# Performance work log

Measured on AMD Instinct MI355X. Metric: run time of the kernel, lower is better.

Reference implementation:

```python
import jax, jax.numpy as jnp
import numpy as np

FS = 16000
NUM_BANDS = 15
CENTER_FREQ = 150
FFT_SIZE = 512
FFT_IN = 256
HOP = 128
NUM_FRAMES = 30
BETA = 1.0 + 10.0 ** (15.0 / 20.0)
FFT_PAD = (FFT_SIZE - FFT_IN) // 2
ROWS = FFT_SIZE // 2 + 1


def _make_fftmat():
    window = np.hanning(FFT_IN)
    window = np.concatenate([np.zeros(FFT_PAD), window, np.zeros(FFT_PAD)])
    fft = np.fft.fft(np.eye(FFT_SIZE))
    fft = np.vstack((np.real(fft[:ROWS, :]), np.imag(fft[:ROWS, :])))
    fft = window * fft  # (2*ROWS, FFT_SIZE)
    return fft.astype(np.float32)


def _make_octmat(fs=FS, nfft=FFT_SIZE, numBands=NUM_BANDS, mn=CENTER_FREQ):
    f = np.linspace(0, fs, nfft + 1)
    f = f[: int(nfft / 2) + 1]
    k = np.arange(float(numBands))
    cf = 2 ** (k / 3) * mn
    fl = np.sqrt(2.0 ** (k / 3) * mn * 2 ** ((k - 1.0) / 3) * mn)
    fr = np.sqrt(2.0 ** (k / 3) * mn * 2 ** ((k + 1.0) / 3) * mn)
    A = np.zeros((numBands, len(f)))
    for i in range(len(cf)):
        b = np.argmin((f - fl[i]) ** 2)
        fl[i] = f[b]
        fl_ii = b
        b = np.argmin((f - fr[i]) ** 2)
        fr[i] = f[b]
        fr_ii = b
        A[i, np.arange(fl_ii, fr_ii)] = 1
    rnk = np.sum(A, axis=1)
    nb = np.where((rnk[1:] >= rnk[:-1]) & (rnk[1:] != 0))[-1][-1] + 1
    A = A[: nb + 1, :]
    return A.astype(np.float32)


def setup_inputs() -> dict:
    key = jax.random.key(0)
    k1, k2, k3 = jax.random.split(key, 3)
    B, L = 64, 128000
    return {
        "prediction": jax.random.normal(k1, (B, L), dtype=jnp.float32),
        "target": jax.random.normal(k2, (B, L), dtype=jnp.float32),
        "inteference": jax.random.normal(k3, (B, L), dtype=jnp.float32),
        "fftmat": jnp.asarray(_make_fftmat()),   # (514, 512)
        "octmat": jnp.asarray(_make_octmat()),   # (n_bands, 257)
    }


def _stft_mag(seq, fftmat):
    # seq: (B, L) -> conv1d with stride HOP, padding FFT_PAD
    out = jax.lax.conv_general_dilated(
        seq[:, None, :], fftmat[:, None, :],
        window_strides=(HOP,), padding=[(FFT_PAD, FFT_PAD)],
        dimension_numbers=("NCH", "OIH", "NCH"))
    real, imag = out[:, :ROWS, :], out[:, ROWS:, :]
    return jnp.sqrt(real ** 2 + imag ** 2)  # (B, ROWS, T)


def _stoi_loss(prediction, target, fftmat, octmat):
    pred_mag = _stft_mag(prediction, fftmat)
    targ_mag = _stft_mag(target, fftmat)
    # octave-band energies: (B, n_bands, T)
    x = jnp.sqrt(jnp.einsum("bft,kf->bkt", targ_mag ** 2, octmat))
    y = jnp.sqrt(jnp.einsum("bft,kf->bkt", pred_mag ** 2, octmat))
    T = x.shape[2]
    W = T - NUM_FRAMES  # windows for m in [NUM_FRAMES, T)
    idx = jnp.arange(W)[:, None] + jnp.arange(NUM_FRAMES)[None, :]  # (W, 30)
    xw = x[:, :, idx]  # (B, K, W, 30)
    yw = y[:, :, idx]
    alpha = jnp.sqrt(jnp.sum(xw ** 2, axis=3, keepdims=True)
                     / (jnp.sum(yw ** 2, axis=3, keepdims=True) + 1e-07))
    yp = jnp.minimum(alpha * yw, BETA * xw)
    xn = xw - jnp.mean(xw, axis=3, keepdims=True)
    xn = xn / jnp.sqrt(jnp.sum(xn ** 2, axis=3, keepdims=True))
    yn = yp - jnp.mean(yp, axis=3, keepdims=True)
    yn = yn / jnp.sqrt(jnp.sum(yn ** 2, axis=3, keepdims=True))
    # per-window correlation: mean over (B, K) of sum over time
    r = jnp.mean(jnp.sum(xn * yn, axis=3), axis=(0, 1))  # (W,)
    return -jnp.sum(r) / W


def reference(prediction, target, inteference, fftmat, octmat):
    return _stoi_loss(prediction, target, fftmat, octmat)
```

## Files before the change

kernel.cpp:

```cpp
#include <hip/hip_runtime.h>
#include <math.h>

#define SIG_L 128000
#define NBATCH 64
#define NROWS 257
#define HOP 128
#define NUMF 999
#define NFRM 30
#define NWIN 969
#define NB_MAX 16
#define FBINS 160
#define TILES 9
#define KSTEPS 16
#define FPB2 128
#define NTC2 8
#define AKB 18432
#define BETA_F 6.623413251903491f

typedef __attribute__((ext_vector_type(8))) short short8;
typedef __attribute__((ext_vector_type(16))) float f32x16;
typedef unsigned short ushort_t;

__device__ inline ushort_t bf_hi_rne(float v, float* rem) {
    unsigned u = __float_as_uint(v);
    unsigned hr = (u + 0x7FFFu + ((u >> 16) & 1u)) & 0xFFFF0000u;
    *rem = v - __uint_as_float(hr);
    return (ushort_t)(hr >> 16);
}
__device__ inline ushort_t bf_rne(float v) {
    unsigned u = __float_as_uint(v);
    return (ushort_t)((u + 0x7FFFu + ((u >> 16) & 1u)) >> 16);
}

__device__ inline void gll16(const void* g, void* l) {
    __builtin_amdgcn_global_load_lds(
        (const __attribute__((address_space(1))) unsigned int*)g,
        (__attribute__((address_space(3))) unsigned int*)l, 16, 0, 0);
}

__global__ void k_scan(const float* __restrict__ oct, int NB, int* __restrict__ hdr) {
    __shared__ int smin[16], smax[16];
    int tid = threadIdx.x;
    if (tid < NB) { smin[tid] = 0x7fffffff; smax[tid] = -1; }
    __syncthreads();
    for (int idx = tid; idx < NB * NROWS; idx += blockDim.x) {
        int k = idx / NROWS, f = idx % NROWS;
        if (oct[idx] != 0.0f) { atomicMin(&smin[k], f); atomicMax(&smax[k], f); }
    }
    __syncthreads();
    if (tid < FBINS) {
        int kid = -1;
        for (int k = 0; k < NB; ++k)
            if (smax[k] >= 0 && tid >= smin[k] && tid <= smax[k]) kid = k;
        hdr[32 + tid] = kid;
    }
}

__global__ void k_prep(const float* __restrict__ fftmat, ushort_t* __restrict__ wpack) {
    for (int u = 0; u < 2; ++u) {
        int idx = blockIdx.x * 512 + u * 256 + threadIdx.x;
        int e = idx & 7, l = (idx >> 3) & 63, p = (idx >> 9) & 1;
        int tt = (idx >> 10) % TILES, kk = (idx >> 10) / TILES;
        int row32 = l & 31, kq = l >> 5;
        int bin = tt * 16 + (row32 >> 1);
        int part = row32 & 1;
        int k = kk * 16 + kq * 8 + e;
        float v = fftmat[(size_t)(part ? (NROWS + bin) : bin) * 512 + 128 + k];
        float rem; ushort_t hb = bf_hi_rne(v, &rem);
        wpack[idx] = p ? bf_rne(rem) : hb;
    }
}

__global__ __launch_bounds__(768, 3) void k_stft(
    const float* __restrict__ targ, const float* __restrict__ pred,
    const ushort_t* __restrict__ wpack, const int* __restrict__ hdr,
    float* __restrict__ xbuf, float* __restrict__ ybuf, int NB) {
    __shared__ __align__(16) char smem[2 * AKB + 65536 + 8192 + 640];
    ushort_t* As    = (ushort_t*)smem;
    ushort_t* Bs    = (ushort_t*)(smem + 2 * AKB);
    float*    bacc  = (float*)(smem + 2 * AKB + 65536);
    int*      kmapS = (int*)(smem + 2 * AKB + 65536 + 8192);

    const int tid = threadIdx.x;
    const int lane = tid & 63;
    const int wv = __builtin_amdgcn_readfirstlane(tid >> 6);
    const int mg  = wv >> 2;
    const int col = (wv >> 1) & 1;
    const int bt  = wv & 1;
    const int tbase = mg * 3;
    const int b = blockIdx.y, z = blockIdx.z;
    const int t0 = blockIdx.x * FPB2;
    const float* __restrict__ sig = z ? pred : targ;
    float* __restrict__ out = z ? ybuf : xbuf;
    const size_t boff = (size_t)b * SIG_L;

    for (int i = tid; i < NB_MAX * FPB2; i += 768) bacc[i] = 0.0f;
    for (int i = tid; i < FBINS; i += 768) kmapS[i] = hdr[32 + i];

    for (int i = tid; i < 4096; i += 768) {
        const int fl = i >> 5, q8 = i & 31;
        const int kk = q8 >> 1, kq = q8 & 1;
        float4 x0 = {0,0,0,0}, x1 = {0,0,0,0};
        if (t0 + fl < NUMF) {
            const float* p = sig + boff + (size_t)(t0 + fl) * HOP + q8 * 8;
            x0 = *(const float4*)(p); x1 = *(const float4*)(p + 4);
        }
        short8 v;
        v[0] = (short)bf_rne(x0.x); v[1] = (short)bf_rne(x0.y);
        v[2] = (short)bf_rne(x0.z); v[3] = (short)bf_rne(x0.w);
        v[4] = (short)bf_rne(x1.x); v[5] = (short)bf_rne(x1.y);
        v[6] = (short)bf_rne(x1.z); v[7] = (short)bf_rne(x1.w);
        *(short8*)&Bs[((kk * 2 + kq) * FPB2 + fl) * 8] = v;
    }
    {
        const char* gsrc = (const char*)wpack;
        for (int j = wv; j < 18; j += 12)
            gll16(gsrc + j * 1024 + lane * 16, smem + j * 1024);
    }
    __syncthreads();

    f32x16 acc0, acc1, acc2;
#pragma unroll
    for (int e = 0; e < 16; ++e) { acc0[e] = 0.0f; acc1[e] = 0.0f; acc2[e] = 0.0f; }

    const int jloc = lane & 31, kq = lane >> 5;
    const int fl = col * 64 + bt * 32 + jloc;

    int cur = 0;
#pragma unroll 1
    for (int kk = 0; kk < KSTEPS; ++kk) {
        if (kk < KSTEPS - 1) {
            const char* gsrc = (const char*)wpack + (size_t)(kk + 1) * AKB;
            char* ldst = smem + (cur ^ 1) * AKB;
            for (int j = wv; j < 18; j += 12)
                gll16(gsrc + j * 1024 + lane * 16, ldst + j * 1024);
        }
        short8 S = *(const short8*)&Bs[((kk * 2 + kq) * FPB2 + fl) * 8];
        const ushort_t* ab = As + cur * (AKB / 2) + tbase * 1024 + lane * 8;
        short8 Ah0 = *(const short8*)(ab);
        short8 Al0 = *(const short8*)(ab + 512);
        short8 Ah1 = *(const short8*)(ab + 1024);
        short8 Al1 = *(const short8*)(ab + 1536);
        short8 Ah2 = *(const short8*)(ab + 2048);
        short8 Al2 = *(const short8*)(ab + 2560);
        __builtin_amdgcn_s_setprio(1);
        acc0 = __builtin_amdgcn_mfma_f32_32x32x16_bf16(Ah0, S, acc0, 0, 0, 0);
        acc1 = __builtin_amdgcn_mfma_f32_32x32x16_bf16(Ah1, S, acc1, 0, 0, 0);
        acc2 = __builtin_amdgcn_mfma_f32_32x32x16_bf16(Ah2, S, acc2, 0, 0, 0);
        acc0 = __builtin_amdgcn_mfma_f32_32x32x16_bf16(Al0, S, acc0, 0, 0, 0);
        acc1 = __builtin_amdgcn_mfma_f32_32x32x16_bf16(Al1, S, acc1, 0, 0, 0);
        acc2 = __builtin_amdgcn_mfma_f32_32x32x16_bf16(Al2, S, acc2, 0, 0, 0);
        __builtin_amdgcn_s_setprio(0);
        __syncthreads();
        cur ^= 1;
    }

    {
        const f32x16* accs[3] = {&acc0, &acc1, &acc2};
#pragma unroll
        for (int g = 0; g < 3; ++g) {
            const f32x16 a = *accs[g];
            float run = 0.0f; int runk = -1;
#pragma unroll
            for (int rr = 0; rr < 8; ++rr) {
                const int m = (rr & 1) + 4 * (rr >> 1) + 2 * kq;
                const int kid = kmapS[(tbase + g) * 16 + m];
                const float vr = a[rr * 2], vi = a[rr * 2 + 1];
                const float e = vr * vr + vi * vi;
                if (kid != runk) {
                    if (runk >= 0) atomicAdd(&bacc[runk * FPB2 + fl], run);
                    run = 0.0f; runk = kid;
                }
                if (kid >= 0) run += e;
            }
            if (runk >= 0) atomicAdd(&bacc[runk * FPB2 + fl], run);
        }
    }
    __syncthreads();
    for (int idx = tid; idx < NB * FPB2; idx += 768) {
        int k = idx >> 7, t = idx & (FPB2 - 1);
        int tg = t0 + t;
        if (tg < NUMF)
            out[((size_t)b * NB + k) * NUMF + tg] = bacc[k * FPB2 + t];
    }
}

__global__ __launch_bounds__(256) void k_corr(const float* __restrict__ xbuf,
                                              const float* __restrict__ ybuf,
                                              int NB, double* __restrict__ partials) {
    const int k = blockIdx.x, b = blockIdx.y;
    const long roff = ((long)b * NB + k) * NUMF;
    __shared__ float xl[NUMF], yl[NUMF];
    __shared__ double red[256];
    const int tid = threadIdx.x;
    for (int i = tid; i < NUMF; i += 256) {
        xl[i] = sqrtf(xbuf[roff + i]);
        yl[i] = sqrtf(ybuf[roff + i]);
    }
    __syncthreads();
    double loc = 0.0;
    for (int w = tid; w < NWIN; w += 256) {
        float sx = 0, sxx = 0, syy = 0;
        for (int i = 0; i < NFRM; ++i) {
            float xv = xl[w + i], yv = yl[w + i];
            sx += xv; sxx += xv * xv; syy += yv * yv;
        }
        float alpha = sqrtf(sxx / (syy + 1e-7f));
        float sy = 0;
        for (int i = 0; i < NFRM; ++i)
            sy += fminf(alpha * yl[w + i], BETA_F * xl[w + i]);
        float mx = sx * (1.0f / NFRM), my = sy * (1.0f / NFRM);
        float cxx = 0, cyy = 0, cxy = 0;
        for (int i = 0; i < NFRM; ++i) {
            float dx = xl[w + i] - mx;
            float dy = fminf(alpha * yl[w + i], BETA_F * xl[w + i]) - my;
            cxx += dx * dx; cyy += dy * dy; cxy += dx * dy;
        }
        loc += (double)cxy / sqrt((double)cxx * (double)cyy);
    }
    red[tid] = loc;
    __syncthreads();
    for (int s = 128; s > 0; s >>= 1) {
        if (tid < s) red[tid] += red[tid + s];
        __syncthreads();
    }
    if (tid == 0) partials[b * NB + k] = red[0];
}

__global__ void k_final(const double* __restrict__ partials, int NB, float* __restrict__ out) {
    __shared__ double red[256];
    const int tid = threadIdx.x;
    const int n = NBATCH * NB;
    double s = 0.0;
    for (int i = tid; i < n; i += 256) s += partials[i];
    red[tid] = s;
    __syncthreads();
    for (int st = 128; st > 0; st >>= 1) {
        if (tid < st) red[tid] += red[tid + st];
        __syncthreads();
    }
    if (tid == 0) out[0] = (float)(-red[0] / ((double)NBATCH * NB * NWIN));
}

extern "C" void kernel_launch(void* const* d_in, const int* in_sizes, int n_in,
                              void* d_out, int out_size, void* d_ws, size_t ws_size,
                              hipStream_t stream) {
    const float* pred   = (const float*)d_in[0];
    const float* targ   = (const float*)d_in[1];
    const float* fftmat = (const float*)d_in[3];
    const float* oct    = (const float*)d_in[4];
    const int NB = in_sizes[4] / NROWS;

    char* ws = (char*)d_ws;
    int*      hdr   = (int*)ws;
    ushort_t* wpack = (ushort_t*)(ws + 1024);
    size_t o1 = 1024 + (size_t)KSTEPS * TILES * 2 * 512 * 2;
    size_t xsz = (size_t)NBATCH * NB_MAX * NUMF * 4;
    float*  xbuf = (float*)(ws + o1);
    float*  ybuf = (float*)(ws + o1 + xsz);
    double* partials = (double*)(ws + o1 + 2 * xsz);

    hipLaunchKernelGGL(k_scan, dim3(1), dim3(256), 0, stream, oct, NB, hdr);
    hipLaunchKernelGGL(k_prep, dim3(288), dim3(256), 0, stream, fftmat, wpack);
    hipLaunchKernelGGL(k_stft, dim3(NTC2, NBATCH, 2), dim3(768), 0, stream,
                       targ, pred, wpack, hdr, xbuf, ybuf, NB);
    hipLaunchKernelGGL(k_corr, dim3(NB, NBATCH), dim3(256), 0, stream, xbuf, ybuf, NB, partials);
    hipLaunchKernelGGL(k_final, dim3(1), dim3(256), 0, stream, partials, NB, (float*)d_out);
}
```

Baseline: 112.4 us.

## Double STFT frames per block and stage contiguous signal chunk in swizzled LDS

Each STFT block now covers 256 frames instead of 128, halving the grid along time. Each wave computes two 32-frame tiles, so every A (weight) fragment loaded from LDS feeds two MFMAs, and the weight stream is fetched by half as many blocks. Because the hop is half the window, the signal is staged once as a contiguous, XOR-swizzled bf16 chunk rather than as duplicated per-frame copies, which cuts global reads and LDS size. The costs are more accumulator registers per wave and fewer blocks (512) to fill the GPU.

```diff
diff --git a/kernel.cpp b/kernel.cpp
--- a/kernel.cpp
+++ b/kernel.cpp
@@ -12,9 +12,10 @@
 #define FBINS 160
 #define TILES 9
 #define KSTEPS 16
-#define FPB2 128
-#define NTC2 8
+#define FPBX 256
+#define NTX 4
 #define AKB 18432
+#define BCH 4112
 #define BETA_F 6.623413251903491f
 
 typedef __attribute__((ext_vector_type(8))) short short8;
@@ -75,42 +76,47 @@
     const float* __restrict__ targ, const float* __restrict__ pred,
     const ushort_t* __restrict__ wpack, const int* __restrict__ hdr,
     float* __restrict__ xbuf, float* __restrict__ ybuf, int NB) {
-    __shared__ __align__(16) char smem[2 * AKB + 65536 + 8192 + 640];
+    __shared__ __align__(16) char smem[2 * AKB + BCH * 16 + NB_MAX * FPBX * 4 + 640];
     ushort_t* As    = (ushort_t*)smem;
-    ushort_t* Bs    = (ushort_t*)(smem + 2 * AKB);
-    float*    bacc  = (float*)(smem + 2 * AKB + 65536);
-    int*      kmapS = (int*)(smem + 2 * AKB + 65536 + 8192);
+    char*     Bs    = smem + 2 * AKB;
+    float*    bacc  = (float*)(smem + 2 * AKB + BCH * 16);
+    int*      kmapS = (int*)(smem + 2 * AKB + BCH * 16 + NB_MAX * FPBX * 4);
 
     const int tid = threadIdx.x;
     const int lane = tid & 63;
     const int wv = __builtin_amdgcn_readfirstlane(tid >> 6);
     const int mg  = wv >> 2;
-    const int col = (wv >> 1) & 1;
-    const int bt  = wv & 1;
+    const int col = wv & 3;
     const int tbase = mg * 3;
     const int b = blockIdx.y, z = blockIdx.z;
-    const int t0 = blockIdx.x * FPB2;
+    const int t0 = blockIdx.x * FPBX;
     const float* __restrict__ sig = z ? pred : targ;
     float* __restrict__ out = z ? ybuf : xbuf;
     const size_t boff = (size_t)b * SIG_L;
 
-    for (int i = tid; i < NB_MAX * FPB2; i += 768) bacc[i] = 0.0f;
+    for (int i = tid; i < NB_MAX * FPBX; i += 768) bacc[i] = 0.0f;
     for (int i = tid; i < FBINS; i += 768) kmapS[i] = hdr[32 + i];
 
-    for (int i = tid; i < 4096; i += 768) {
-        const int fl = i >> 5, q8 = i & 31;
-        const int kk = q8 >> 1, kq = q8 & 1;
-        float4 x0 = {0,0,0,0}, x1 = {0,0,0,0};
-        if (t0 + fl < NUMF) {
-            const float* p = sig + boff + (size_t)(t0 + fl) * HOP + q8 * 8;
-            x0 = *(const float4*)(p); x1 = *(const float4*)(p + 4);
-        }
-        short8 v;
-        v[0] = (short)bf_rne(x0.x); v[1] = (short)bf_rne(x0.y);
-        v[2] = (short)bf_rne(x0.z); v[3] = (short)bf_rne(x0.w);
-        v[4] = (short)bf_rne(x1.x); v[5] = (short)bf_rne(x1.y);
-        v[6] = (short)bf_rne(x1.z); v[7] = (short)bf_rne(x1.w);
-        *(short8*)&Bs[((kk * 2 + kq) * FPB2 + fl) * 8] = v;
+    const long sbase = (long)t0 * HOP;
+    for (int c = tid; c < BCH; c += 768) {
+        const long g0 = sbase + (long)c * 8;
+        float v[8];
+        if (g0 + 8 <= SIG_L) {
+            float4 x0 = *(const float4*)(sig + boff + g0);
+            float4 x1 = *(const float4*)(sig + boff + g0 + 4);
+            v[0] = x0.x; v[1] = x0.y; v[2] = x0.z; v[3] = x0.w;
+            v[4] = x1.x; v[5] = x1.y; v[6] = x1.z; v[7] = x1.w;
+        } else {
+#pragma unroll
+            for (int e = 0; e < 8; ++e)
+                v[e] = (g0 + e < SIG_L) ? sig[boff + g0 + e] : 0.0f;
+        }
+        short8 sv;
+#pragma unroll
+        for (int e = 0; e < 8; ++e) sv[e] = (short)bf_rne(v[e]);
+        int byte = c * 16;
+        byte ^= ((byte >> 8) & 0xF) << 4;
+        *(short8*)(Bs + byte) = sv;
     }
     {
         const char* gsrc = (const char*)wpack;
@@ -119,12 +125,15 @@
     }
     __syncthreads();
 
-    f32x16 acc0, acc1, acc2;
-#pragma unroll
-    for (int e = 0; e < 16; ++e) { acc0[e] = 0.0f; acc1[e] = 0.0f; acc2[e] = 0.0f; }
+    f32x16 acc[3][2];
+#pragma unroll
+    for (int g = 0; g < 3; ++g)
+#pragma unroll
+        for (int bt = 0; bt < 2; ++bt)
+#pragma unroll
+            for (int e = 0; e < 16; ++e) acc[g][bt][e] = 0.0f;
 
     const int jloc = lane & 31, kq = lane >> 5;
-    const int fl = col * 64 + bt * 32 + jloc;
 
     int cur = 0;
 #pragma unroll 1
@@ -135,53 +144,57 @@
             for (int j = wv; j < 18; j += 12)
                 gll16(gsrc + j * 1024 + lane * 16, ldst + j * 1024);
         }
-        short8 S = *(const short8*)&Bs[((kk * 2 + kq) * FPB2 + fl) * 8];
+        short8 S[2];
+#pragma unroll
+        for (int bt = 0; bt < 2; ++bt) {
+            const int fl = col * 64 + bt * 32 + jloc;
+            int byte = fl * 256 + kk * 32 + kq * 16;
+            byte ^= ((byte >> 8) & 0xF) << 4;
+            S[bt] = *(const short8*)(Bs + byte);
+        }
         const ushort_t* ab = As + cur * (AKB / 2) + tbase * 1024 + lane * 8;
-        short8 Ah0 = *(const short8*)(ab);
-        short8 Al0 = *(const short8*)(ab + 512);
-        short8 Ah1 = *(const short8*)(ab + 1024);
-        short8 Al1 = *(const short8*)(ab + 1536);
-        short8 Ah2 = *(const short8*)(ab + 2048);
-        short8 Al2 = *(const short8*)(ab + 2560);
         __builtin_amdgcn_s_setprio(1);
-        acc0 = __builtin_amdgcn_mfma_f32_32x32x16_bf16(Ah0, S, acc0, 0, 0, 0);
-        acc1 = __builtin_amdgcn_mfma_f32_32x32x16_bf16(Ah1, S, acc1, 0, 0, 0);
-        acc2 = __builtin_amdgcn_mfma_f32_32x32x16_bf16(Ah2, S, acc2, 0, 0, 0);
-        acc0 = __builtin_amdgcn_mfma_f32_32x32x16_bf16(Al0, S, acc0, 0, 0, 0);
-        acc1 = __builtin_amdgcn_mfma_f32_32x32x16_bf16(Al1, S, acc1, 0, 0, 0);
-        acc2 = __builtin_amdgcn_mfma_f32_32x32x16_bf16(Al2, S, acc2, 0, 0, 0);
+#pragma unroll
+        for (int g = 0; g < 3; ++g) {
+            short8 Ah = *(const short8*)(ab + g * 1024);
+            short8 Al = *(const short8*)(ab + g * 1024 + 512);
+            acc[g][0] = __builtin_amdgcn_mfma_f32_32x32x16_bf16(Ah, S[0], acc[g][0], 0, 0, 0);
+            acc[g][1] = __builtin_amdgcn_mfma_f32_32x32x16_bf16(Ah, S[1], acc[g][1], 0, 0, 0);
+            acc[g][0] = __builtin_amdgcn_mfma_f32_32x32x16_bf16(Al, S[0], acc[g][0], 0, 0, 0);
+            acc[g][1] = __builtin_amdgcn_mfma_f32_32x32x16_bf16(Al, S[1], acc[g][1], 0, 0, 0);
+        }
         __builtin_amdgcn_s_setprio(0);
         __syncthreads();
         cur ^= 1;
     }
 
-    {
-        const f32x16* accs[3] = {&acc0, &acc1, &acc2};
-#pragma unroll
-        for (int g = 0; g < 3; ++g) {
-            const f32x16 a = *accs[g];
+#pragma unroll
+    for (int g = 0; g < 3; ++g) {
+#pragma unroll
+        for (int bt = 0; bt < 2; ++bt) {
+            const int fl = col * 64 + bt * 32 + jloc;
             float run = 0.0f; int runk = -1;
 #pragma unroll
             for (int rr = 0; rr < 8; ++rr) {
                 const int m = (rr & 1) + 4 * (rr >> 1) + 2 * kq;
                 const int kid = kmapS[(tbase + g) * 16 + m];
-                const float vr = a[rr * 2], vi = a[rr * 2 + 1];
+                const float vr = acc[g][bt][rr * 2], vi = acc[g][bt][rr * 2 + 1];
                 const float e = vr * vr + vi * vi;
                 if (kid != runk) {
-                    if (runk >= 0) atomicAdd(&bacc[runk * FPB2 + fl], run);
+                    if (runk >= 0) atomicAdd(&bacc[runk * FPBX + fl], run);
                     run = 0.0f; runk = kid;
                 }
                 if (kid >= 0) run += e;
             }
-            if (runk >= 0) atomicAdd(&bacc[runk * FPB2 + fl], run);
-        }
-    }
-    __syncthreads();
-    for (int idx = tid; idx < NB * FPB2; idx += 768) {
-        int k = idx >> 7, t = idx & (FPB2 - 1);
+            if (runk >= 0) atomicAdd(&bacc[runk * FPBX + fl], run);
+        }
+    }
+    __syncthreads();
+    for (int idx = tid; idx < NB * FPBX; idx += 768) {
+        int k = idx >> 8, t = idx & (FPBX - 1);
         int tg = t0 + t;
         if (tg < NUMF)
-            out[((size_t)b * NB + k) * NUMF + tg] = bacc[k * FPB2 + t];
+            out[((size_t)b * NB + k) * NUMF + tg] = bacc[k * FPBX + t];
     }
 }
 
@@ -262,7 +275,7 @@
 
     hipLaunchKernelGGL(k_scan, dim3(1), dim3(256), 0, stream, oct, NB, hdr);
     hipLaunchKernelGGL(k_prep, dim3(288), dim3(256), 0, stream, fftmat, wpack);
-    hipLaunchKernelGGL(k_stft, dim3(NTC2, NBATCH, 2), dim3(768), 0, stream,
+    hipLaunchKernelGGL(k_stft, dim3(NTX, NBATCH, 2), dim3(768), 0, stream,
                        targ, pred, wpack, hdr, xbuf, ybuf, NB);
     hipLaunchKernelGGL(k_corr, dim3(NB, NBATCH), dim3(256), 0, stream, xbuf, ybuf, NB, partials);
     hipLaunchKernelGGL(k_final, dim3(1), dim3(256), 0, stream, partials, NB, (float*)d_out);
```

Result: faster. 103.7 us (-7.7%).
